# Optimization experiments

Hardware: AMD Instinct MI355X
Metric: run time of the kernel (lower is better)

## Reference

```python
import jax, jax.numpy as jnp
import numpy as np
from jax import lax

N = 524288
HID = 20
IN = 2


def setup_inputs() -> dict:
    key = jax.random.key(0)
    ks = jax.random.split(key, 12)
    s = 1.0 / np.sqrt(HID)  # PyTorch LSTM init scale
    inp = {
        "gradients": jax.random.normal(ks[0], (N,), dtype=jnp.float32),
        "parameters": jax.random.normal(ks[1], (N,), dtype=jnp.float32),
        # layer 0 (input_size=2)
        "W_ih0": jax.random.uniform(ks[2], (4 * HID, IN), jnp.float32, -s, s),
        "W_hh0": jax.random.uniform(ks[3], (4 * HID, HID), jnp.float32, -s, s),
        "b_ih0": jax.random.uniform(ks[4], (4 * HID,), jnp.float32, -s, s),
        "b_hh0": jax.random.uniform(ks[5], (4 * HID,), jnp.float32, -s, s),
        # layer 1 (input_size=HID)
        "W_ih1": jax.random.uniform(ks[6], (4 * HID, HID), jnp.float32, -s, s),
        "W_hh1": jax.random.uniform(ks[7], (4 * HID, HID), jnp.float32, -s, s),
        "b_ih1": jax.random.uniform(ks[8], (4 * HID,), jnp.float32, -s, s),
        "b_hh1": jax.random.uniform(ks[9], (4 * HID,), jnp.float32, -s, s),
        # output head Linear(HID, 1)
        "W_out": jax.random.uniform(ks[10], (1, HID), jnp.float32, -s, s),
        "b_out": jax.random.uniform(ks[11], (1,), jnp.float32, -s, s),
    }
    return inp


def _lstm_layer(x, W_ih, W_hh, b_ih, b_hh):
    # x: [T, D_in] -> hidden sequence [T, H]; PyTorch gate order i,f,g,o.
    H = W_hh.shape[1]
    # Input projection for all timesteps in one GEMM (hoisted out of scan).
    gx = x @ W_ih.T + (b_ih + b_hh)  # [T, 4H]

    def step(carry, g_t):
        h, c = carry
        g = g_t + h @ W_hh.T  # [4H]
        i, f, gg, o = jnp.split(g, 4)
        i = jax.nn.sigmoid(i)
        f = jax.nn.sigmoid(f)
        gg = jnp.tanh(gg)
        o = jax.nn.sigmoid(o)
        c = f * c + i * gg
        h = o * jnp.tanh(c)
        return (h, c), h

    h0 = jnp.zeros((H,), x.dtype)
    c0 = jnp.zeros((H,), x.dtype)
    _, hs = lax.scan(step, (h0, c0), gx)
    return hs  # [T, H]


def reference(gradients, parameters, W_ih0, W_hh0, b_ih0, b_hh0,
              W_ih1, W_hh1, b_ih1, b_hh1, W_out, b_out):
    x = jnp.stack([gradients, parameters], axis=-1)  # [N, 2]
    h1 = _lstm_layer(x, W_ih0, W_hh0, b_ih0, b_hh0)   # [N, H]
    h2 = _lstm_layer(h1, W_ih1, W_hh1, b_ih1, b_hh1)  # [N, H]
    update = h2 @ W_out.T + b_out                      # [N, 1]
    return update[:, 0]                                # [N]
```

## Files before the change

kernel.cpp:

```cpp
#include <hip/hip_runtime.h>

#define HIDN 20
#define CHUNK 256
#define WARM 64
#define NB ((CHUNK + WARM) / 64)
#define WARMB (WARM / 64)

typedef float v2f __attribute__((ext_vector_type(2)));

__device__ __forceinline__ float bcast(float v, int l) {
    return __int_as_float(__builtin_amdgcn_readlane(__float_as_int(v), l));
}
__device__ __forceinline__ v2f fma2(v2f a, v2f b, v2f c) {
    return __builtin_elementwise_fma(a, b, c);
}

__device__ __forceinline__ float gate_update(float aA, float aB, float& c,
                                             float cA, float mA, float dA,
                                             bool hB) {
    const float cB = -1.4426950408889634f;
    const float cT =  2.8853900817779268f;
    float eA = __builtin_amdgcn_exp2f(cA * aA);
    float sA = __builtin_amdgcn_rcpf(1.0f + eA);
    float gA = __builtin_fmaf(mA, sA, -dA);
    float eB = __builtin_amdgcn_exp2f(cB * aB);
    float gB = __builtin_amdgcn_rcpf(1.0f + eB);
    float oA = __shfl_xor(gA, 32);
    float oB = __shfl_xor(gB, 32);
    float f = hB ? oB : gB;
    float o = hB ? gB : oB;
    c = __builtin_fmaf(f, c, gA * oA);
    float ec = __builtin_amdgcn_exp2f(cT * c);
    float tc = 1.0f - 2.0f * __builtin_amdgcn_rcpf(ec + 1.0f);
    return o * tc;
}

#define RJA(M) M(0) M(1) M(2) M(3) M(4)
#define RJB(M) M(5) M(6) M(7) M(8) M(9)
#define RJ(M) RJA(M) RJB(M)

__global__ __launch_bounds__(64)
__attribute__((amdgpu_waves_per_eu(2, 2)))
void lstm_opt_kernel(const float* __restrict__ grad, const float* __restrict__ par,
                     const float* __restrict__ Wih0, const float* __restrict__ Whh0,
                     const float* __restrict__ bih0, const float* __restrict__ bhh0,
                     const float* __restrict__ Wih1, const float* __restrict__ Whh1,
                     const float* __restrict__ bih1, const float* __restrict__ bhh1,
                     const float* __restrict__ Wout, const float* __restrict__ bout,
                     float* __restrict__ out, int n)
{
    __shared__ __align__(16) float hbuf[40];

    const int lane  = threadIdx.x;
    const int lh    = lane & 31;
    const bool hB   = lane >= 32;
    const int u     = (lh < HIDN) ? lh : (HIDN - 1);
    const bool valid = (lh < HIDN);

    const int rowA = (hB ? 2 : 0) * HIDN + u;
    const int rowB = (hB ? 3 : 1) * HIDN + u;

#define DECLW(j) v2f w0A_##j, w0B_##j, wiA_##j, wiB_##j, whA_##j, whB_##j;
    RJ(DECLW)
#undef DECLW
#define LOADW(j) \
    w0A_##j.x = Whh0[rowA * HIDN + 2*j]; w0A_##j.y = Whh0[rowA * HIDN + 2*j + 1]; \
    w0B_##j.x = Whh0[rowB * HIDN + 2*j]; w0B_##j.y = Whh0[rowB * HIDN + 2*j + 1]; \
    wiA_##j.x = Wih1[rowA * HIDN + 2*j]; wiA_##j.y = Wih1[rowA * HIDN + 2*j + 1]; \
    wiB_##j.x = Wih1[rowB * HIDN + 2*j]; wiB_##j.y = Wih1[rowB * HIDN + 2*j + 1]; \
    whA_##j.x = Whh1[rowA * HIDN + 2*j]; whA_##j.y = Whh1[rowA * HIDN + 2*j + 1]; \
    whB_##j.x = Whh1[rowB * HIDN + 2*j]; whB_##j.y = Whh1[rowB * HIDN + 2*j + 1];
    RJ(LOADW)
#undef LOADW

    float wxAg = Wih0[rowA * 2 + 0], wxAp = Wih0[rowA * 2 + 1];
    float wxBg = Wih0[rowB * 2 + 0], wxBp = Wih0[rowB * 2 + 1];
    float bA0 = bih0[rowA] + bhh0[rowA];
    float bB0 = bih0[rowB] + bhh0[rowB];
    float bA1 = bih1[rowA] + bhh1[rowA];
    float bB1 = bih1[rowB] + bhh1[rowB];
    float wo = valid ? Wout[u] : 0.f;
    const float bo = bout[0];

#define PINW(j) asm volatile("" : "+v"(w0A_##j), "+v"(w0B_##j), "+v"(wiA_##j), \
                                  "+v"(wiB_##j), "+v"(whA_##j), "+v"(whB_##j));
    RJ(PINW)
#undef PINW
    asm volatile("" : "+v"(wxAg), "+v"(wxAp), "+v"(wxBg), "+v"(wxBp));
    asm volatile("" : "+v"(bA0), "+v"(bB0), "+v"(bA1), "+v"(bB1), "+v"(wo));

    const float mA = hB ? 2.0f : 1.0f;
    const float dA = hB ? 1.0f : 0.0f;
    const float cA = -1.4426950408889634f * mA;

    float c0 = 0.f, c1 = 0.f;

    const int t0     = blockIdx.x * CHUNK;
    const int tstart = t0 - WARM;

    float xgv, xpv;
    { int ti = tstart + lane; ti = ti < 0 ? 0 : ti; xgv = grad[ti]; xpv = par[ti]; }

    {
        const float xg0 = bcast(xgv, 0), xp0 = bcast(xpv, 0);
        const float pA = __builtin_fmaf(wxAp, xp0, __builtin_fmaf(wxAg, xg0, bA0));
        const float pB = __builtin_fmaf(wxBp, xp0, __builtin_fmaf(wxBg, xg0, bB0));
        c0 = 0.f;
        const float h0i = gate_update(pA, pB, c0, cA, mA, dA, hB);
        hbuf[u] = h0i;
        hbuf[HIDN + u] = 0.f;
        c1 = 0.f;
    }

    float rbuf = 0.f;

#pragma unroll 1
    for (int b = 0; b < NB; ++b) {
        float xgn = 0.f, xpn = 0.f;
        if (b + 1 < NB) {
            int ti = tstart + (b + 1) * 64 + lane;
            ti = ti < 0 ? 0 : (ti >= n ? n - 1 : ti);
            xgn = grad[ti]; xpn = par[ti];
        }
        if (b == WARMB && blockIdx.x == 0) {
            const float xg0 = bcast(xgv, 0), xp0 = bcast(xpv, 0);
            const float pA = __builtin_fmaf(wxAp, xp0, __builtin_fmaf(wxAg, xg0, bA0));
            const float pB = __builtin_fmaf(wxBp, xp0, __builtin_fmaf(wxBg, xg0, bB0));
            c0 = 0.f;
            const float h0i = gate_update(pA, pB, c0, cA, mA, dA, hB);
            hbuf[u] = h0i;
            hbuf[HIDN + u] = 0.f;
            c1 = 0.f;
        }
        const bool main_phase = (b >= WARMB);

#pragma unroll 2
        for (int j = 0; j < 64; ++j) {
            const int ln = (j + 1) & 63;
            const float xgN = bcast((j < 63) ? xgv : xgn, ln);
            const float xpN = bcast((j < 63) ? xpv : xpn, ln);

            v2f hp0_0, hp0_1, hp0_2, hp0_3, hp0_4, hp0_5, hp0_6, hp0_7, hp0_8, hp0_9;
            v2f hp1_0, hp1_1, hp1_2, hp1_3, hp1_4, hp1_5, hp1_6, hp1_7, hp1_8, hp1_9;
            {
                const float4 r0 = *reinterpret_cast<const float4*>(&hbuf[0]);
                const float4 r1 = *reinterpret_cast<const float4*>(&hbuf[4]);
                const float4 r2 = *reinterpret_cast<const float4*>(&hbuf[8]);
                const float4 r3 = *reinterpret_cast<const float4*>(&hbuf[12]);
                const float4 r4 = *reinterpret_cast<const float4*>(&hbuf[16]);
                hp0_0.x = r0.x; hp0_0.y = r0.y;  hp0_1.x = r0.z; hp0_1.y = r0.w;
                hp0_2.x = r1.x; hp0_2.y = r1.y;  hp0_3.x = r1.z; hp0_3.y = r1.w;
                hp0_4.x = r2.x; hp0_4.y = r2.y;  hp0_5.x = r2.z; hp0_5.y = r2.w;
                hp0_6.x = r3.x; hp0_6.y = r3.y;  hp0_7.x = r3.z; hp0_7.y = r3.w;
                hp0_8.x = r4.x; hp0_8.y = r4.y;  hp0_9.x = r4.z; hp0_9.y = r4.w;
                const float4 s0 = *reinterpret_cast<const float4*>(&hbuf[20]);
                const float4 s1 = *reinterpret_cast<const float4*>(&hbuf[24]);
                const float4 s2 = *reinterpret_cast<const float4*>(&hbuf[28]);
                const float4 s3 = *reinterpret_cast<const float4*>(&hbuf[32]);
                const float4 s4 = *reinterpret_cast<const float4*>(&hbuf[36]);
                hp1_0.x = s0.x; hp1_0.y = s0.y;  hp1_1.x = s0.z; hp1_1.y = s0.w;
                hp1_2.x = s1.x; hp1_2.y = s1.y;  hp1_3.x = s1.z; hp1_3.y = s1.w;
                hp1_4.x = s2.x; hp1_4.y = s2.y;  hp1_5.x = s2.z; hp1_5.y = s2.w;
                hp1_6.x = s3.x; hp1_6.y = s3.y;  hp1_7.x = s3.z; hp1_7.y = s3.w;
                hp1_8.x = s4.x; hp1_8.y = s4.y;  hp1_9.x = s4.z; hp1_9.y = s4.w;
            }

            v2f qA = {0.f, 0.f}, qB = {0.f, 0.f}, qA2 = {0.f, 0.f}, qB2 = {0.f, 0.f};
#define F1A(j_) qA  = fma2(wiA_##j_, hp0_##j_, qA);  qB  = fma2(wiB_##j_, hp0_##j_, qB);
#define F1B(j_) qA2 = fma2(whA_##j_, hp1_##j_, qA2); qB2 = fma2(whB_##j_, hp1_##j_, qB2);
            RJ(F1A) RJ(F1B)
#undef F1A
#undef F1B

            v2f aA = {0.f, 0.f}, aB = {0.f, 0.f}, aA2 = {0.f, 0.f}, aB2 = {0.f, 0.f};
#define F0A(j_) aA  = fma2(w0A_##j_, hp0_##j_, aA);  aB  = fma2(w0B_##j_, hp0_##j_, aB);
#define F0B(j_) aA2 = fma2(w0A_##j_, hp0_##j_, aA2); aB2 = fma2(w0B_##j_, hp0_##j_, aB2);
            RJA(F0A) RJB(F0B)
#undef F0A
#undef F0B

            const float a1A = ((qA.x + qA.y) + (qA2.x + qA2.y)) + bA1;
            const float a1B = ((qB.x + qB.y) + (qB2.x + qB2.y)) + bB1;
            const float xpA = __builtin_fmaf(wxAp, xpN, __builtin_fmaf(wxAg, xgN, bA0));
            const float xpB = __builtin_fmaf(wxBp, xpN, __builtin_fmaf(wxBg, xgN, bB0));
            const float a0A = ((aA.x + aA.y) + (aA2.x + aA2.y)) + xpA;
            const float a0B = ((aB.x + aB.y) + (aB2.x + aB2.y)) + xpB;

            const float h1cur  = gate_update(a1A, a1B, c1, cA, mA, dA, hB);
            const float h0next = gate_update(a0A, a0B, c0, cA, mA, dA, hB);

            hbuf[u] = h0next;
            hbuf[HIDN + u] = h1cur;

            if (main_phase) {
                float p = h1cur * wo;
                p += __shfl_xor(p, 16);
                p += __shfl_xor(p, 8);
                p += __shfl_xor(p, 4);
                p += __shfl_xor(p, 2);
                p += __shfl_xor(p, 1);
                rbuf = (lane == j) ? (p + bo) : rbuf;
            }
        }
        if (main_phase) {
            int t = tstart + b * 64 + lane;
            if (t >= 0 && t < n) out[t] = rbuf;
        }
        xgv = xgn; xpv = xpn;
    }
}

extern "C" void kernel_launch(void* const* d_in, const int* in_sizes, int n_in,
                              void* d_out, int out_size, void* d_ws, size_t ws_size,
                              hipStream_t stream) {
    const float* grad = (const float*)d_in[0];
    const float* par  = (const float*)d_in[1];
    const float* Wih0 = (const float*)d_in[2];
    const float* Whh0 = (const float*)d_in[3];
    const float* bih0 = (const float*)d_in[4];
    const float* bhh0 = (const float*)d_in[5];
    const float* Wih1 = (const float*)d_in[6];
    const float* Whh1 = (const float*)d_in[7];
    const float* bih1 = (const float*)d_in[8];
    const float* bhh1 = (const float*)d_in[9];
    const float* Wout = (const float*)d_in[10];
    const float* bout = (const float*)d_in[11];
    float* out = (float*)d_out;

    const int n = in_sizes[0];
    const int chunks = (n + CHUNK - 1) / CHUNK;

    lstm_opt_kernel<<<chunks, 64, 0, stream>>>(grad, par, Wih0, Whh0, bih0, bhh0,
                                               Wih1, Whh1, bih1, bhh1, Wout, bout,
                                               out, n);
}
```

Before: 229.8 us.

## Defer output head reduction to LDS and use permlane32 swap for half exchange

Each timestep's output-head partial products are written to a 64x24 shared array. One vectorized row-sum per 64-step block then replaces the per-step 5-level shuffle reduction inside the serial recurrence. The cross-half gate exchange uses the permlane32_swap builtin when available instead of a ds_bpermute-based shuffle. Both changes aim to shorten the critical latency chain of each sequential step, at the cost of extra LDS stores per step and added shared memory.

```diff
diff --git a/kernel.cpp b/kernel.cpp
--- a/kernel.cpp
+++ b/kernel.cpp
@@ -7,12 +7,22 @@
 #define WARMB (WARM / 64)
 
 typedef float v2f __attribute__((ext_vector_type(2)));
+typedef unsigned int v2u __attribute__((ext_vector_type(2)));
 
 __device__ __forceinline__ float bcast(float v, int l) {
     return __int_as_float(__builtin_amdgcn_readlane(__float_as_int(v), l));
 }
 __device__ __forceinline__ v2f fma2(v2f a, v2f b, v2f c) {
     return __builtin_elementwise_fma(a, b, c);
+}
+__device__ __forceinline__ float xchg32(float g) {
+#if __has_builtin(__builtin_amdgcn_permlane32_swap)
+    const unsigned int gu = __float_as_uint(g);
+    const v2u r = __builtin_amdgcn_permlane32_swap(gu, gu, false, false);
+    return __uint_as_float(r.x ^ r.y ^ gu);
+#else
+    return __shfl_xor(g, 32);
+#endif
 }
 
 __device__ __forceinline__ float gate_update(float aA, float aB, float& c,
@@ -25,8 +35,8 @@
     float gA = __builtin_fmaf(mA, sA, -dA);
     float eB = __builtin_amdgcn_exp2f(cB * aB);
     float gB = __builtin_amdgcn_rcpf(1.0f + eB);
-    float oA = __shfl_xor(gA, 32);
-    float oB = __shfl_xor(gB, 32);
+    float oA = xchg32(gA);
+    float oB = xchg32(gB);
     float f = hB ? oB : gB;
     float o = hB ? gB : oB;
     c = __builtin_fmaf(f, c, gA * oA);
@@ -50,12 +60,14 @@
                      float* __restrict__ out, int n)
 {
     __shared__ __align__(16) float hbuf[40];
+    __shared__ __align__(16) float hstore[64][24];
 
     const int lane  = threadIdx.x;
     const int lh    = lane & 31;
     const bool hB   = lane >= 32;
     const int u     = (lh < HIDN) ? lh : (HIDN - 1);
     const bool valid = (lh < HIDN);
+    const int wcol  = valid ? lh : (HIDN + (lane & 3));
 
     const int rowA = (hB ? 2 : 0) * HIDN + u;
     const int rowB = (hB ? 3 : 1) * HIDN + u;
@@ -111,8 +123,6 @@
         hbuf[HIDN + u] = 0.f;
         c1 = 0.f;
     }
-
-    float rbuf = 0.f;
 
 #pragma unroll 1
     for (int b = 0; b < NB; ++b) {
@@ -192,19 +202,22 @@
             hbuf[u] = h0next;
             hbuf[HIDN + u] = h1cur;
 
-            if (main_phase) {
-                float p = h1cur * wo;
-                p += __shfl_xor(p, 16);
-                p += __shfl_xor(p, 8);
-                p += __shfl_xor(p, 4);
-                p += __shfl_xor(p, 2);
-                p += __shfl_xor(p, 1);
-                rbuf = (lane == j) ? (p + bo) : rbuf;
-            }
-        }
+            hstore[j][wcol] = h1cur * wo;
+        }
+
         if (main_phase) {
+            const float4 a0 = *reinterpret_cast<const float4*>(&hstore[lane][0]);
+            const float4 a1 = *reinterpret_cast<const float4*>(&hstore[lane][4]);
+            const float4 a2 = *reinterpret_cast<const float4*>(&hstore[lane][8]);
+            const float4 a3 = *reinterpret_cast<const float4*>(&hstore[lane][12]);
+            const float4 a4 = *reinterpret_cast<const float4*>(&hstore[lane][16]);
+            float s = (((a0.x + a0.y) + (a0.z + a0.w)) +
+                       ((a1.x + a1.y) + (a1.z + a1.w))) +
+                      (((a2.x + a2.y) + (a2.z + a2.w)) +
+                       ((a3.x + a3.y) + (a3.z + a3.w))) +
+                      ((a4.x + a4.y) + (a4.z + a4.w));
             int t = tstart + b * 64 + lane;
-            if (t >= 0 && t < n) out[t] = rbuf;
+            if (t >= 0 && t < n) out[t] = s + bo;
         }
         xgv = xgn; xpv = xpn;
     }
```

New measurement: 211.5 us. -8.0%, faster.
